# Kernel optimization log

Measured on AMD Instinct MI355X. Metric: run time of the kernel, lower is better.

The kernel has to match this reference:

```python
import jax, jax.numpy as jnp
import numpy as np

B, C, H, W = 1, 320, 64, 64
HEADS, DH = 8, 40            # inner_dim = 320
CTX_LEN, CTX_DIM = 77, 768
FF_MULT = 4
GN_GROUPS, GN_EPS = 32, 1e-6
LN_EPS = 1e-5
SCALE = DH ** -0.5
WSTD = 0.02


def setup_inputs() -> dict:
    key = jax.random.key(0)
    ks = iter(jax.random.split(key, 32))
    rn = lambda *s: jax.random.normal(next(ks), s, dtype=jnp.float32)
    D = HEADS * DH  # 320
    inp = {
        'hidden_states': rn(B, C, H, W),
        'encoder_hidden_states': rn(B, CTX_LEN, CTX_DIM),
        'gn_g': jnp.ones((C,), jnp.float32), 'gn_b': jnp.zeros((C,), jnp.float32),
        'pi_w': rn(C, D) * WSTD, 'pi_b': jnp.zeros((D,), jnp.float32),
        'n1_g': jnp.ones((D,), jnp.float32), 'n1_b': jnp.zeros((D,), jnp.float32),
        'a1_q': rn(D, D) * WSTD, 'a1_k': rn(D, D) * WSTD, 'a1_v': rn(D, D) * WSTD,
        'a1_o': rn(D, D) * WSTD, 'a1_ob': jnp.zeros((D,), jnp.float32),
        'n2_g': jnp.ones((D,), jnp.float32), 'n2_b': jnp.zeros((D,), jnp.float32),
        'a2_q': rn(D, D) * WSTD, 'a2_k': rn(CTX_DIM, D) * WSTD, 'a2_v': rn(CTX_DIM, D) * WSTD,
        'a2_o': rn(D, D) * WSTD, 'a2_ob': jnp.zeros((D,), jnp.float32),
        'n3_g': jnp.ones((D,), jnp.float32), 'n3_b': jnp.zeros((D,), jnp.float32),
        'ff_w1': rn(D, 2 * FF_MULT * D) * WSTD, 'ff_b1': jnp.zeros((2 * FF_MULT * D,), jnp.float32),
        'ff_w2': rn(FF_MULT * D, D) * WSTD, 'ff_b2': jnp.zeros((D,), jnp.float32),
        'po_w': rn(D, C) * WSTD, 'po_b': jnp.zeros((C,), jnp.float32),
    }
    return inp


def _group_norm(x, g, b):
    # x: [B,C,H,W]
    Bx, Cx, Hx, Wx = x.shape
    xr = x.reshape(Bx, GN_GROUPS, Cx // GN_GROUPS, Hx, Wx)
    mu = xr.mean(axis=(2, 3, 4), keepdims=True)
    var = xr.var(axis=(2, 3, 4), keepdims=True)
    xr = (xr - mu) * jax.lax.rsqrt(var + GN_EPS)
    x = xr.reshape(Bx, Cx, Hx, Wx)
    return x * g[None, :, None, None] + b[None, :, None, None]


def _layer_norm(x, g, b):
    mu = x.mean(-1, keepdims=True)
    var = x.var(-1, keepdims=True)
    return (x - mu) * jax.lax.rsqrt(var + LN_EPS) * g + b


def _attention(x, ctx, wq, wk, wv, wo, bo):
    # x: [B,S,D]; ctx: [B,T,Dc]. Same math as the torch sliced loop
    # (the 2-row slicing changes only execution order, not values).
    Bx, S, D = x.shape
    q = (x @ wq).reshape(Bx, S, HEADS, DH)
    k = (ctx @ wk).reshape(Bx, -1, HEADS, DH)
    v = (ctx @ wv).reshape(Bx, -1, HEADS, DH)
    s = jnp.einsum('bihd,bjhd->bhij', q, k) * SCALE
    p = jax.nn.softmax(s, axis=-1)
    o = jnp.einsum('bhij,bjhd->bihd', p, v).reshape(Bx, S, D)
    return o @ wo + bo


def reference(hidden_states, encoder_hidden_states, gn_g, gn_b, pi_w, pi_b,
              n1_g, n1_b, a1_q, a1_k, a1_v, a1_o, a1_ob,
              n2_g, n2_b, a2_q, a2_k, a2_v, a2_o, a2_ob,
              n3_g, n3_b, ff_w1, ff_b1, ff_w2, ff_b2, po_w, po_b):
    residual = hidden_states
    h = _group_norm(hidden_states, gn_g, gn_b)
    # proj_in: 1x1 conv == per-pixel linear; to [B, HW, D]
    h = jnp.einsum('bchw,cd->bhwd', h, pi_w) + pi_b
    Bx, Hx, Wx, D = h.shape
    h = h.reshape(Bx, Hx * Wx, D)

    # transformer block
    nh = _layer_norm(h, n1_g, n1_b)
    h = h + _attention(nh, nh, a1_q, a1_k, a1_v, a1_o, a1_ob)
    nh = _layer_norm(h, n2_g, n2_b)
    h = h + _attention(nh, encoder_hidden_states, a2_q, a2_k, a2_v, a2_o, a2_ob)
    nh = _layer_norm(h, n3_g, n3_b)
    hg = nh @ ff_w1 + ff_b1
    a, gate = jnp.split(hg, 2, axis=-1)  # GEGLU
    h = h + (a * jax.nn.gelu(gate, approximate=False)) @ ff_w2 + ff_b2

    # proj_out 1x1 conv then residual
    h = h.reshape(Bx, Hx, Wx, D)
    out = jnp.einsum('bhwd,dc->bchw', h, po_w) + po_b[None, :, None, None]
    return out + residual
```

## Files before the change

### kernel.cpp

```cpp
#include <hip/hip_runtime.h>

typedef __bf16 bf16x8 __attribute__((ext_vector_type(8)));
typedef __bf16 bf16x4 __attribute__((ext_vector_type(4)));
typedef __bf16 bf16x2 __attribute__((ext_vector_type(2)));
typedef float f32x4 __attribute__((ext_vector_type(4)));
typedef float f32x16 __attribute__((ext_vector_type(16)));

#define MFMA16(a, b, c) __builtin_amdgcn_mfma_f32_16x16x32_bf16(a, b, c, 0, 0, 0)
#define MFMA32(a, b, c) __builtin_amdgcn_mfma_f32_32x32x16_bf16(a, b, c, 0, 0, 0)

static constexpr float QSCALE = 0.15811388300841897f * 1.4426950408889634f;

__device__ __forceinline__ void gload16(const __bf16* g, __bf16* l) {
  __builtin_amdgcn_global_load_lds((const __attribute__((address_space(1))) void*)g,
                                   (__attribute__((address_space(3))) void*)l, 16, 0, 0);
}

__device__ __forceinline__ bf16x8 zero8() {
  bf16x8 z;
#pragma unroll
  for (int j = 0; j < 8; ++j) z[j] = (__bf16)0.0f;
  return z;
}

__device__ __forceinline__ float gelu_exact(float x) {
  return 0.5f * x * (1.0f + erff(x * 0.70710678118654752f));
}

__device__ __forceinline__ int vslot(int kk) {
  int G = kk >> 5, klo = kk & 31;
  int m = (klo >> 4) & 1, hik = (klo >> 2) & 1;
  int jj = (klo & 3) | (((klo >> 3) & 1) << 2);
  return (G << 5) | (m << 4) | (hik << 3) | jj;
}

struct WDesc { const float* src; __bf16* dst; int K; int N; int ldn; int noff; };
struct WTable { WDesc w[12]; };

__global__ __launch_bounds__(256) void wconv_kernel(WTable tab) {
  WDesc d = tab.w[blockIdx.y];
  int total = (d.K >> 3) * d.N;
  int idx = blockIdx.x * 256 + threadIdx.x;
  if (idx >= total) return;
  int kb = idx / d.N, n = idx - kb * d.N;
  bf16x8 o;
#pragma unroll
  for (int j = 0; j < 8; ++j) o[j] = (__bf16)d.src[(size_t)(kb * 8 + j) * d.N + n];
  *(bf16x8*)&d.dst[((size_t)kb * d.ldn + d.noff + n) * 8] = o;
}

__global__ __launch_bounds__(256) void gn_stats(const float* __restrict__ X,
                                                float* __restrict__ part) {
  int g = blockIdx.x >> 3, cid = blockIdx.x & 7;
  const float* base = X + (size_t)g * 40960 + (size_t)cid * 5120;
  int t = threadIdx.x;
  float s = 0.f, s2 = 0.f;
#pragma unroll
  for (int i = t; i < 1280; i += 256) {
    float4 v = ((const float4*)base)[i];
    s += v.x + v.y + v.z + v.w;
    s2 += v.x * v.x + v.y * v.y + v.z * v.z + v.w * v.w;
  }
#pragma unroll
  for (int off = 1; off < 64; off <<= 1) { s += __shfl_xor(s, off); s2 += __shfl_xor(s2, off); }
  __shared__ float rs[4], rs2[4];
  int wid = t >> 6, lane = t & 63;
  if (lane == 0) { rs[wid] = s; rs2[wid] = s2; }
  __syncthreads();
  if (t == 0) {
    part[blockIdx.x * 2] = rs[0] + rs[1] + rs[2] + rs[3];
    part[blockIdx.x * 2 + 1] = rs2[0] + rs2[1] + rs2[2] + rs2[3];
  }
}

__global__ __launch_bounds__(256) void gn_apply(const float* __restrict__ X,
                                                const float* __restrict__ part,
                                                const float* __restrict__ gg,
                                                const float* __restrict__ gb,
                                                __bf16* __restrict__ Y) {
  int i0 = (blockIdx.x * 256 + threadIdx.x) * 8;
  int c = i0 >> 12, px = i0 & 4095;
  int g = c / 10;
  float s = 0.f, s2 = 0.f;
#pragma unroll
  for (int j = 0; j < 8; ++j) { s += part[(g * 8 + j) * 2]; s2 += part[(g * 8 + j) * 2 + 1]; }
  float mu = s * (1.f / 40960.f);
  float rstd = rsqrtf(s2 * (1.f / 40960.f) - mu * mu + 1e-6f);
  float ga = gg[c] * rstd, bb = gb[c] - mu * ga;
  float4 a = *(const float4*)&X[i0];
  float4 b = *(const float4*)&X[i0 + 4];
  Y[(size_t)(px + 0) * 320 + c] = (__bf16)(a.x * ga + bb);
  Y[(size_t)(px + 1) * 320 + c] = (__bf16)(a.y * ga + bb);
  Y[(size_t)(px + 2) * 320 + c] = (__bf16)(a.z * ga + bb);
  Y[(size_t)(px + 3) * 320 + c] = (__bf16)(a.w * ga + bb);
  Y[(size_t)(px + 4) * 320 + c] = (__bf16)(b.x * ga + bb);
  Y[(size_t)(px + 5) * 320 + c] = (__bf16)(b.y * ga + bb);
  Y[(size_t)(px + 6) * 320 + c] = (__bf16)(b.z * ga + bb);
  Y[(size_t)(px + 7) * 320 + c] = (__bf16)(b.w * ga + bb);
}

__global__ __launch_bounds__(256) void ln_kernel(const float* __restrict__ X,
                                                 const float* __restrict__ g,
                                                 const float* __restrict__ b,
                                                 __bf16* __restrict__ Y) {
  int row = blockIdx.x * 4 + (threadIdx.x >> 6);
  int lane = threadIdx.x & 63;
  const float* x = X + (size_t)row * 320;
  float v[5];
  float s = 0.f;
#pragma unroll
  for (int i = 0; i < 5; ++i) { v[i] = x[lane + 64 * i]; s += v[i]; }
#pragma unroll
  for (int off = 1; off < 64; off <<= 1) s += __shfl_xor(s, off);
  float mu = s * (1.f / 320.f);
  float s2 = 0.f;
#pragma unroll
  for (int i = 0; i < 5; ++i) { float d = v[i] - mu; s2 += d * d; }
#pragma unroll
  for (int off = 1; off < 64; off <<= 1) s2 += __shfl_xor(s2, off);
  float rstd = rsqrtf(s2 * (1.f / 320.f) + 1e-5f);
#pragma unroll
  for (int i = 0; i < 5; ++i) {
    int c = lane + 64 * i;
    Y[(size_t)row * 320 + c] = (__bf16)((v[i] - mu) * rstd * g[c] + b[c]);
  }
}

template <int OM, bool HB, bool HR, bool QS, bool AH>
__global__ __launch_bounds__(256) void gemm64(const __bf16* __restrict__ A,
                                              const __bf16* __restrict__ Bt,
                                              const float* __restrict__ bias,
                                              const float* __restrict__ res,
                                              void* __restrict__ Cout,
                                              void* __restrict__ Cout2,
                                              int M, int N, int K) {
  __shared__ __align__(16) __bf16 sA[2][4096];
  __shared__ __align__(16) __bf16 sB[2][4096];
  int t = threadIdx.x, lane = t & 63, wid = t >> 6;
  int wr = wid >> 1, wc = wid & 1, kb4 = lane >> 4, l15 = lane & 15;
  int m0 = blockIdx.x * 64, n0 = blockIdx.y * 64;
  const size_t N8 = (size_t)N * 8;
  f32x4 acc[2][2] = {};
  int r0 = t >> 3, c0 = (t & 7) ^ (r0 & 7);

  auto stage = [&](int buf, int k0) {
    const __bf16 *ga0, *ga1;
    if (AH) {
      int kk = k0 + c0 * 8;
      int hh = kk / 40, dh = kk - hh * 40;
      ga0 = &A[((size_t)hh * 4096 + m0 + r0) * 40 + dh];
      ga1 = &A[((size_t)hh * 4096 + m0 + 32 + r0) * 40 + dh];
    } else {
      ga0 = &A[(size_t)(m0 + r0) * K + k0 + c0 * 8];
      ga1 = &A[(size_t)(m0 + 32 + r0) * K + k0 + c0 * 8];
    }
    gload16(ga0, &sA[buf][wid * 512]);
    gload16(ga1, &sA[buf][2048 + wid * 512]);
    gload16(&Bt[((size_t)(k0 >> 3) + wid) * N8 + (size_t)(n0 + lane) * 8], &sB[buf][wid * 512]);
    gload16(&Bt[((size_t)(k0 >> 3) + wid + 4) * N8 + (size_t)(n0 + lane) * 8], &sB[buf][2048 + wid * 512]);
  };
  stage(0, 0);
  __syncthreads();
  int cur = 0;
  for (int k0 = 0; k0 < K; k0 += 64) {
    if (k0 + 64 < K) stage(cur ^ 1, k0 + 64);
#pragma unroll
    for (int kk = 0; kk < 2; ++kk) {
      int c8 = kb4 + kk * 4;
      bf16x8 af[2], bfr[2];
#pragma unroll
      for (int fm = 0; fm < 2; ++fm) {
        int row = wr * 32 + fm * 16 + l15;
        af[fm] = *(const bf16x8*)&sA[cur][row * 64 + ((c8 * 8) ^ ((row & 7) << 3))];
      }
#pragma unroll
      for (int fn = 0; fn < 2; ++fn)
        bfr[fn] = *(const bf16x8*)&sB[cur][(c8 * 64 + wc * 32 + fn * 16 + l15) * 8];
#pragma unroll
      for (int fm = 0; fm < 2; ++fm)
#pragma unroll
        for (int fn = 0; fn < 2; ++fn) acc[fm][fn] = MFMA16(af[fm], bfr[fn], acc[fm][fn]);
    }
    __syncthreads();
    cur ^= 1;
  }
#pragma unroll
  for (int fm = 0; fm < 2; ++fm)
#pragma unroll
    for (int fn = 0; fn < 2; ++fn)
#pragma unroll
      for (int r = 0; r < 4; ++r) {
        int row = m0 + wr * 32 + fm * 16 + kb4 * 4 + r;
        int col = n0 + wc * 32 + fn * 16 + l15;
        float v = acc[fm][fn][r];
        if (HB) v += bias[col];
        if (OM == 3) {
          if (HR) v += res[(size_t)col * M + row];
          ((float*)Cout)[(size_t)col * M + row] = v;
        } else if (OM == 4) {
          int hh = col / 40, dh = col - hh * 40;
          __bf16* qp = (__bf16*)Cout + ((size_t)hh * 4096 + row) * 48 + dh;
          *qp = (__bf16)(QS ? v * QSCALE : v);
          if (dh >= 32) qp[8] = (__bf16)0.f;
        } else {
          if (HR) v += res[(size_t)row * N + col];
          if (OM == 0) {
            ((float*)Cout)[(size_t)row * N + col] = v;
          } else if (OM == 1) {
            ((__bf16*)Cout)[(size_t)row * N + col] = (__bf16)(QS ? v * QSCALE : v);
          } else {
            ((float*)Cout)[(size_t)row * N + col] = v;
            ((__bf16*)Cout2)[(size_t)row * N + col] = (__bf16)v;
          }
        }
      }
}

__global__ __launch_bounds__(256) void qkv_gemm(const __bf16* __restrict__ A,
                                                const __bf16* __restrict__ Bt,
                                                __bf16* __restrict__ Qh,
                                                __bf16* __restrict__ Khp,
                                                __bf16* __restrict__ Vtl) {
  __shared__ __align__(16) __bf16 sA[2][4096];
  __shared__ __align__(16) __bf16 sB[2][4096];
  int t = threadIdx.x, lane = t & 63, wid = t >> 6;
  int wr = wid >> 1, wc = wid & 1, kb4 = lane >> 4, l15 = lane & 15;
  int m0 = blockIdx.x * 64, n0 = blockIdx.y * 64;
  f32x4 acc[2][2] = {};
  int r0 = t >> 3, c0 = (t & 7) ^ (r0 & 7);

  auto stage = [&](int buf, int k0) {
    gload16(&A[(size_t)(m0 + r0) * 320 + k0 + c0 * 8], &sA[buf][wid * 512]);
    gload16(&A[(size_t)(m0 + 32 + r0) * 320 + k0 + c0 * 8], &sA[buf][2048 + wid * 512]);
    gload16(&Bt[((size_t)(k0 >> 3) + wid) * (960 * 8) + (size_t)(n0 + lane) * 8], &sB[buf][wid * 512]);
    gload16(&Bt[((size_t)(k0 >> 3) + wid + 4) * (960 * 8) + (size_t)(n0 + lane) * 8], &sB[buf][2048 + wid * 512]);
  };
  stage(0, 0);
  __syncthreads();
  int cur = 0;
  for (int k0 = 0; k0 < 320; k0 += 64) {
    if (k0 + 64 < 320) stage(cur ^ 1, k0 + 64);
#pragma unroll
    for (int kk = 0; kk < 2; ++kk) {
      int c8 = kb4 + kk * 4;
      bf16x8 af[2], bfr[2];
#pragma unroll
      for (int fm = 0; fm < 2; ++fm) {
        int row = wr * 32 + fm * 16 + l15;
        af[fm] = *(const bf16x8*)&sA[cur][row * 64 + ((c8 * 8) ^ ((row & 7) << 3))];
      }
#pragma unroll
      for (int fn = 0; fn < 2; ++fn)
        bfr[fn] = *(const bf16x8*)&sB[cur][(c8 * 64 + wc * 32 + fn * 16 + l15) * 8];
#pragma unroll
      for (int fm = 0; fm < 2; ++fm)
#pragma unroll
        for (int fn = 0; fn < 2; ++fn) acc[fm][fn] = MFMA16(af[fm], bfr[fn], acc[fm][fn]);
    }
    __syncthreads();
    cur ^= 1;
  }
#pragma unroll
  for (int fm = 0; fm < 2; ++fm)
#pragma unroll
    for (int fn = 0; fn < 2; ++fn)
#pragma unroll
      for (int r = 0; r < 4; ++r) {
        int row = m0 + wr * 32 + fm * 16 + kb4 * 4 + r;
        int col = n0 + wc * 32 + fn * 16 + l15;
        float v = acc[fm][fn][r];
        if (col < 320) {
          int hh = col / 40, dh = col - hh * 40;
          __bf16* qp = &Qh[((size_t)hh * 4096 + row) * 48 + dh];
          *qp = (__bf16)(v * QSCALE);
          if (dh >= 32) qp[8] = (__bf16)0.f;
        } else if (col < 640) {
          int d = col - 320;
          int hh = d / 40, dh = d - hh * 40;
          __bf16* kp = &Khp[((size_t)hh * 4096 + row) * 48 + dh];
          *kp = (__bf16)v;
          if (dh >= 32) kp[8] = (__bf16)0.f;
        } else {
          int d = col - 640;
          int hh = d / 40, dh = d - hh * 40;
          int kt = row >> 6;
          int slot = vslot(row & 63);
          int cidx = (slot & 7) | ((((slot >> 3) ^ dh) & 7) << 3);
          Vtl[(((size_t)hh * 64 + kt) * 40 + dh) * 64 + cidx] = (__bf16)v;
        }
      }
}

__global__ __launch_bounds__(256) void kv2_gemm(const float* __restrict__ Af,
                                                const __bf16* __restrict__ Bt,
                                                __bf16* __restrict__ Khp,
                                                __bf16* __restrict__ Vtl) {
  __shared__ __align__(16) __bf16 sA[2][4][64][8];
  __shared__ __align__(16) __bf16 sB[2][4][64][8];
  int t = threadIdx.x, lane = t & 63, wid = t >> 6;
  int wr = wid >> 1, wc = wid & 1, kb4 = lane >> 4, l15 = lane & 15;
  int m0 = blockIdx.x * 64, n0 = blockIdx.y * 64;
  int am = t & 63, ac8 = t >> 6;
  int bn = t & 63, bkb = t >> 6;
  f32x4 acc[2][2] = {};
  bf16x8 rA, rB;
  auto loadA = [&](int k0) -> bf16x8 {
    if (m0 + am < 77) {
      const float* src = &Af[(size_t)(m0 + am) * 768 + k0 + ac8 * 8];
      float4 x = *(const float4*)src;
      float4 y = *(const float4*)(src + 4);
      bf16x8 o;
      o[0] = (__bf16)x.x; o[1] = (__bf16)x.y; o[2] = (__bf16)x.z; o[3] = (__bf16)x.w;
      o[4] = (__bf16)y.x; o[5] = (__bf16)y.y; o[6] = (__bf16)y.z; o[7] = (__bf16)y.w;
      return o;
    }
    return zero8();
  };
  auto loadB = [&](int k0) {
    return *(const bf16x8*)&Bt[((size_t)(k0 >> 3) + bkb) * (640 * 8) + (size_t)(n0 + bn) * 8];
  };
  rA = loadA(0); rB = loadB(0);
  *(bf16x8*)&sA[0][ac8][am][0] = rA;
  *(bf16x8*)&sB[0][bkb][bn][0] = rB;
  __syncthreads();
  int cur = 0;
  for (int k0 = 0; k0 < 768; k0 += 32, cur ^= 1) {
    bool more = (k0 + 32) < 768;
    if (more) { rA = loadA(k0 + 32); rB = loadB(k0 + 32); }
    bf16x8 af[2], bfr[2];
#pragma unroll
    for (int fm = 0; fm < 2; ++fm) af[fm] = *(const bf16x8*)&sA[cur][kb4][wr * 32 + fm * 16 + l15][0];
#pragma unroll
    for (int fn = 0; fn < 2; ++fn) bfr[fn] = *(const bf16x8*)&sB[cur][kb4][wc * 32 + fn * 16 + l15][0];
#pragma unroll
    for (int fm = 0; fm < 2; ++fm)
#pragma unroll
      for (int fn = 0; fn < 2; ++fn) acc[fm][fn] = MFMA16(af[fm], bfr[fn], acc[fm][fn]);
    if (more) {
      *(bf16x8*)&sA[cur ^ 1][ac8][am][0] = rA;
      *(bf16x8*)&sB[cur ^ 1][bkb][bn][0] = rB;
    }
    __syncthreads();
  }
#pragma unroll
  for (int fm = 0; fm < 2; ++fm)
#pragma unroll
    for (int fn = 0; fn < 2; ++fn)
#pragma unroll
      for (int r = 0; r < 4; ++r) {
        int row = m0 + wr * 32 + fm * 16 + kb4 * 4 + r;
        int col = n0 + wc * 32 + fn * 16 + l15;
        float v = acc[fm][fn][r];
        if (col < 320) {
          int hh = col / 40, dh = col - hh * 40;
          __bf16* kp = &Khp[((size_t)hh * 128 + row) * 48 + dh];
          *kp = (__bf16)v;
          if (dh >= 32) kp[8] = (__bf16)0.f;
        } else {
          int d = col - 320;
          int hh = d / 40, dh = d - hh * 40;
          int kt = row >> 6;
          int slot = vslot(row & 63);
          int cidx = (slot & 7) | ((((slot >> 3) ^ dh) & 7) << 3);
          Vtl[(((size_t)hh * 2 + kt) * 40 + dh) * 64 + cidx] = (__bf16)v;
        }
      }
}

__global__ __launch_bounds__(256) void geglu64(const __bf16* __restrict__ A,
                                               const __bf16* __restrict__ Bt,
                                               const float* __restrict__ bias,
                                               __bf16* __restrict__ Out) {
  __shared__ __align__(16) __bf16 sA[2][4096];
  __shared__ __align__(16) __bf16 sB[2][4096];
  __shared__ __align__(16) __bf16 sBg[2][4096];
  int t = threadIdx.x, lane = t & 63, wid = t >> 6;
  int wr = wid >> 1, wc = wid & 1, kb4 = lane >> 4, l15 = lane & 15;
  int m0 = blockIdx.x * 64, n0 = blockIdx.y * 64;
  f32x4 acc_a[2][2] = {}, acc_g[2][2] = {};
  int r0 = t >> 3, c0 = (t & 7) ^ (r0 & 7);

  auto stage = [&](int buf, int k0) {
    gload16(&A[(size_t)(m0 + r0) * 320 + k0 + c0 * 8], &sA[buf][wid * 512]);
    gload16(&A[(size_t)(m0 + 32 + r0) * 320 + k0 + c0 * 8], &sA[buf][2048 + wid * 512]);
    gload16(&Bt[((size_t)(k0 >> 3) + wid) * (2560 * 8) + (size_t)(n0 + lane) * 8], &sB[buf][wid * 512]);
    gload16(&Bt[((size_t)(k0 >> 3) + wid + 4) * (2560 * 8) + (size_t)(n0 + lane) * 8], &sB[buf][2048 + wid * 512]);
    gload16(&Bt[((size_t)(k0 >> 3) + wid) * (2560 * 8) + (size_t)(1280 + n0 + lane) * 8], &sBg[buf][wid * 512]);
    gload16(&Bt[((size_t)(k0 >> 3) + wid + 4) * (2560 * 8) + (size_t)(1280 + n0 + lane) * 8], &sBg[buf][2048 + wid * 512]);
  };
  stage(0, 0);
  __syncthreads();
  int cur = 0;
  for (int k0 = 0; k0 < 320; k0 += 64) {
    if (k0 + 64 < 320) stage(cur ^ 1, k0 + 64);
#pragma unroll
    for (int kk = 0; kk < 2; ++kk) {
      int c8 = kb4 + kk * 4;
      bf16x8 af[2], bfa[2], bfg[2];
#pragma unroll
      for (int fm = 0; fm < 2; ++fm) {
        int row = wr * 32 + fm * 16 + l15;
        af[fm] = *(const bf16x8*)&sA[cur][row * 64 + ((c8 * 8) ^ ((row & 7) << 3))];
      }
#pragma unroll
      for (int fn = 0; fn < 2; ++fn) {
        bfa[fn] = *(const bf16x8*)&sB[cur][(c8 * 64 + wc * 32 + fn * 16 + l15) * 8];
        bfg[fn] = *(const bf16x8*)&sBg[cur][(c8 * 64 + wc * 32 + fn * 16 + l15) * 8];
      }
#pragma unroll
      for (int fm = 0; fm < 2; ++fm)
#pragma unroll
        for (int fn = 0; fn < 2; ++fn) {
          acc_a[fm][fn] = MFMA16(af[fm], bfa[fn], acc_a[fm][fn]);
          acc_g[fm][fn] = MFMA16(af[fm], bfg[fn], acc_g[fm][fn]);
        }
    }
    __syncthreads();
    cur ^= 1;
  }
#pragma unroll
  for (int fm = 0; fm < 2; ++fm)
#pragma unroll
    for (int fn = 0; fn < 2; ++fn)
#pragma unroll
      for (int r = 0; r < 4; ++r) {
        int row = m0 + wr * 32 + fm * 16 + kb4 * 4 + r;
        int col = n0 + wc * 32 + fn * 16 + l15;
        float a = acc_a[fm][fn][r] + bias[col];
        float g = acc_g[fm][fn][r] + bias[1280 + col];
        Out[(size_t)row * 1280 + col] = (__bf16)(a * gelu_exact(g));
      }
}

__global__ __launch_bounds__(512) void attn_kernel(const __bf16* __restrict__ Qh,
                                                   const __bf16* __restrict__ Khp,
                                                   const __bf16* __restrict__ Vtl,
                                                   __bf16* __restrict__ Oh,
                                                   int kv_len, int kvpad) {
  __shared__ __align__(16) char smem[48128];
  int t = threadIdx.x, lane = t & 63, wid = t >> 6;
  int zz = wid >> 2, kg = (wid >> 1) & 1, qg = wid & 1;
  int tl = t & 255, wv = wid & 3;
  int l31 = lane & 31, hi = lane >> 5;
  int h = blockIdx.y, q0 = blockIdx.x * 64;
  int q = q0 + qg * 32 + l31;
  int NT = kvpad >> 6;
  char* zbase = smem + zz * 22528;
  __bf16* sK  = (__bf16*)zbase;
  __bf16* sVs = (__bf16*)(zbase + 12288);
  __bf16* sVc = (__bf16*)(smem + 45056);
  for (int i = t; i < 1536; i += 512) sVc[i] = (i < 64) ? (__bf16)1.0f : (__bf16)0.0f;

  const __bf16* Kb = Khp + (size_t)h * kvpad * 48;
  const __bf16* Vb = Vtl + (size_t)h * NT * 2560;

  bf16x8 qf[3];
  {
    const __bf16* qrow = Qh + ((size_t)h * 4096 + q) * 48;
#pragma unroll
    for (int s = 0; s < 3; ++s) qf[s] = *(const bf16x8*)(qrow + s * 16 + hi * 8);
  }
  f32x16 o_lo = {}, o_hi = {};

  auto stage = [&](int buf, int k0) {
    const __bf16* kgp = Kb + (size_t)k0 * 48;
    __bf16* kd = sK + buf * 3072;
    gload16(kgp + tl * 8, kd + wv * 512);
    if (tl < 128) gload16(kgp + 2048 + tl * 8, kd + 2048 + wv * 512);
    const __bf16* vgp = Vb + (size_t)(k0 >> 6) * 2560;
    __bf16* vd = sVs + buf * 2560;
    gload16(vgp + tl * 8, vd + wv * 512);
    if (tl < 64) gload16(vgp + 2048 + tl * 8, vd + 2048);
  };

  int span = kvpad >> 1;
  int kstart = zz * span, ntl = span >> 6;
  stage(0, kstart);
  __syncthreads();
  int d7 = l31 & 7;
  for (int tile = 0; tile < ntl; ++tile) {
    int k0 = kstart + (tile << 6), cur = tile & 1;
    if (tile + 1 < ntl) stage(cur ^ 1, k0 + 64);
    const __bf16* K8 = sK + cur * 3072 + (kg * 32 + l31) * 48 + hi * 8;
    f32x16 s = {};
#pragma unroll
    for (int sl = 0; sl < 3; ++sl) {
      bf16x8 kf = *(const bf16x8*)(K8 + sl * 16);
      s = MFMA32(kf, qf[sl], s);
    }
    if (k0 + 64 > kv_len) {
#pragma unroll
      for (int r = 0; r < 16; ++r) {
        int klo = (r & 3) + 8 * (r >> 2) + 4 * hi;
        if (k0 + kg * 32 + klo >= kv_len) s[r] = -1e30f;
      }
    }
    bf16x8 p0, p1;
#pragma unroll
    for (int j = 0; j < 8; ++j) {
      p0[j] = (__bf16)exp2f(s[j]);
      p1[j] = (__bf16)exp2f(s[8 + j]);
    }
    const __bf16* Vlo = sVs + cur * 2560 + l31 * 64;
    const __bf16* Vhi = (l31 < 8) ? (sVs + cur * 2560 + (32 + l31) * 64)
                                  : (sVc + (l31 - 8) * 64);
#pragma unroll
    for (int m = 0; m < 2; ++m) {
      int blk = (4 * kg + 2 * m + hi) ^ d7;
      bf16x8 vlo = *(const bf16x8*)(Vlo + blk * 8);
      bf16x8 vhi = *(const bf16x8*)(Vhi + blk * 8);
      bf16x8 pm = (m == 0) ? p0 : p1;
      o_lo = MFMA32(vlo, pm, o_lo);
      o_hi = MFMA32(vhi, pm, o_hi);
    }
    __syncthreads();
  }
  float* sO = (float*)smem;
  int srcid = zz * 2 + kg;
  if (srcid != 0) {
    float* dst = sO + (((size_t)qg * 3 + (srcid - 1)) * 64 + lane) * 24;
#pragma unroll
    for (int r = 0; r < 16; ++r) dst[r] = o_lo[r];
#pragma unroll
    for (int r = 0; r < 4; ++r) dst[16 + r] = o_hi[r];
    dst[20] = o_hi[4];
  }
  __syncthreads();
  if (srcid == 0) {
#pragma unroll
    for (int src = 0; src < 3; ++src) {
      const float* sp = sO + (((size_t)qg * 3 + src) * 64 + lane) * 24;
#pragma unroll
      for (int r = 0; r < 16; ++r) o_lo[r] += sp[r];
#pragma unroll
      for (int r = 0; r < 4; ++r) o_hi[r] += sp[16 + r];
      o_hi[4] += sp[20];
    }
    float ls = __shfl(o_hi[4], l31);
    float inv = 1.0f / ls;
    __bf16* orow = Oh + ((size_t)h * 4096 + q) * 40;
#pragma unroll
    for (int r = 0; r < 16; r += 2) {
      int d = (r & 3) + 8 * (r >> 2) + 4 * hi;
      bf16x2 o2;
      o2[0] = (__bf16)(o_lo[r] * inv);
      o2[1] = (__bf16)(o_lo[r + 1] * inv);
      *(bf16x2*)(orow + d) = o2;
    }
#pragma unroll
    for (int r = 0; r < 4; r += 2) {
      int d = 32 + r + 4 * hi;
      bf16x2 o2;
      o2[0] = (__bf16)(o_hi[r] * inv);
      o2[1] = (__bf16)(o_hi[r + 1] * inv);
      *(bf16x2*)(orow + d) = o2;
    }
  }
}

extern "C" void kernel_launch(void* const* d_in, const int* in_sizes, int n_in,
                              void* d_out, int out_size, void* d_ws, size_t ws_size,
                              hipStream_t stream) {
  const float* hs    = (const float*)d_in[0];
  const float* ctx   = (const float*)d_in[1];
  const float* gn_g  = (const float*)d_in[2];
  const float* gn_b  = (const float*)d_in[3];
  const float* pi_w  = (const float*)d_in[4];
  const float* pi_b  = (const float*)d_in[5];
  const float* n1_g  = (const float*)d_in[6];
  const float* n1_b  = (const float*)d_in[7];
  const float* a1_q  = (const float*)d_in[8];
  const float* a1_k  = (const float*)d_in[9];
  const float* a1_v  = (const float*)d_in[10];
  const float* a1_o  = (const float*)d_in[11];
  const float* a1_ob = (const float*)d_in[12];
  const float* n2_g  = (const float*)d_in[13];
  const float* n2_b  = (const float*)d_in[14];
  const float* a2_q  = (const float*)d_in[15];
  const float* a2_k  = (const float*)d_in[16];
  const float* a2_v  = (const float*)d_in[17];
  const float* a2_o  = (const float*)d_in[18];
  const float* a2_ob = (const float*)d_in[19];
  const float* n3_g  = (const float*)d_in[20];
  const float* n3_b  = (const float*)d_in[21];
  const float* ff_w1 = (const float*)d_in[22];
  const float* ff_b1 = (const float*)d_in[23];
  const float* ff_w2 = (const float*)d_in[24];
  const float* ff_b2 = (const float*)d_in[25];
  const float* po_w  = (const float*)d_in[26];
  const float* po_b  = (const float*)d_in[27];

  char* p = (char*)d_ws;
  auto alloc = [&](size_t bytes) {
    char* r = p;
    p += (bytes + 255) & ~(size_t)255;
    return r;
  };
  __bf16* wPI  = (__bf16*)alloc((size_t)320 * 320 * 2);
  __bf16* wQKV = (__bf16*)alloc((size_t)320 * 960 * 2);
  __bf16* wO1  = (__bf16*)alloc((size_t)320 * 320 * 2);
  __bf16* wQ2  = (__bf16*)alloc((size_t)320 * 320 * 2);
  __bf16* wKV2 = (__bf16*)alloc((size_t)768 * 640 * 2);
  __bf16* wO2  = (__bf16*)alloc((size_t)320 * 320 * 2);
  __bf16* wFF1 = (__bf16*)alloc((size_t)320 * 2560 * 2);
  __bf16* wFF2 = (__bf16*)alloc((size_t)1280 * 320 * 2);
  __bf16* wPO  = (__bf16*)alloc((size_t)320 * 320 * 2);

  float*  gpart= (float*)alloc((size_t)256 * 2 * 4);
  __bf16* xg   = (__bf16*)alloc((size_t)4096 * 320 * 2);
  float*  h    = (float*)alloc((size_t)4096 * 320 * 4);
  __bf16* hb   = (__bf16*)alloc((size_t)4096 * 320 * 2);
  __bf16* nx   = (__bf16*)alloc((size_t)4096 * 320 * 2);
  __bf16* qh   = (__bf16*)alloc((size_t)8 * 4096 * 48 * 2);
  __bf16* khp  = (__bf16*)alloc((size_t)8 * 4096 * 48 * 2);
  __bf16* vtl  = (__bf16*)alloc((size_t)8 * 64 * 2560 * 2);
  __bf16* kh2  = (__bf16*)alloc((size_t)8 * 128 * 48 * 2);
  __bf16* vt2  = (__bf16*)alloc((size_t)8 * 2 * 2560 * 2);
  __bf16* oh   = (__bf16*)alloc((size_t)4096 * 320 * 2);
  __bf16* g    = (__bf16*)alloc((size_t)4096 * 1280 * 2);
  float*  outp = (float*)d_out;

  WTable tab;
  tab.w[0]  = WDesc{pi_w,  wPI,  320, 320, 320, 0};
  tab.w[1]  = WDesc{a1_q,  wQKV, 320, 320, 960, 0};
  tab.w[2]  = WDesc{a1_k,  wQKV, 320, 320, 960, 320};
  tab.w[3]  = WDesc{a1_v,  wQKV, 320, 320, 960, 640};
  tab.w[4]  = WDesc{a1_o,  wO1,  320, 320, 320, 0};
  tab.w[5]  = WDesc{a2_q,  wQ2,  320, 320, 320, 0};
  tab.w[6]  = WDesc{a2_k,  wKV2, 768, 320, 640, 0};
  tab.w[7]  = WDesc{a2_v,  wKV2, 768, 320, 640, 320};
  tab.w[8]  = WDesc{a2_o,  wO2,  320, 320, 320, 0};
  tab.w[9]  = WDesc{ff_w1, wFF1, 320, 2560, 2560, 0};
  tab.w[10] = WDesc{ff_w2, wFF2, 1280, 320, 320, 0};
  tab.w[11] = WDesc{po_w,  wPO,  320, 320, 320, 0};
  wconv_kernel<<<dim3(400, 12), 256, 0, stream>>>(tab);
  gn_stats<<<dim3(256), 256, 0, stream>>>(hs, gpart);
  gn_apply<<<dim3(640), 256, 0, stream>>>(hs, gpart, gn_g, gn_b, xg);
  gemm64<0, true, false, false, false><<<dim3(64, 5), 256, 0, stream>>>(xg, wPI, pi_b, nullptr, h, nullptr, 4096, 320, 320);
  ln_kernel<<<dim3(1024), 256, 0, stream>>>(h, n1_g, n1_b, nx);
  qkv_gemm<<<dim3(64, 15), 256, 0, stream>>>(nx, wQKV, qh, khp, vtl);
  attn_kernel<<<dim3(64, 8), 512, 0, stream>>>(qh, khp, vtl, oh, 4096, 4096);
  gemm64<0, true, true, false, true><<<dim3(64, 5), 256, 0, stream>>>(oh, wO1, a1_ob, h, h, nullptr, 4096, 320, 320);
  ln_kernel<<<dim3(1024), 256, 0, stream>>>(h, n2_g, n2_b, nx);
  gemm64<4, false, false, true, false><<<dim3(64, 5), 256, 0, stream>>>(nx, wQ2, nullptr, nullptr, qh, nullptr, 4096, 320, 320);
  kv2_gemm<<<dim3(2, 10), 256, 0, stream>>>(ctx, wKV2, kh2, vt2);
  attn_kernel<<<dim3(64, 8), 512, 0, stream>>>(qh, kh2, vt2, oh, 77, 128);
  gemm64<0, true, true, false, true><<<dim3(64, 5), 256, 0, stream>>>(oh, wO2, a2_ob, h, h, nullptr, 4096, 320, 320);
  ln_kernel<<<dim3(1024), 256, 0, stream>>>(h, n3_g, n3_b, nx);
  geglu64<<<dim3(64, 20), 256, 0, stream>>>(nx, wFF1, ff_b1, g);
  gemm64<2, true, true, false, false><<<dim3(64, 5), 256, 0, stream>>>(g, wFF2, ff_b2, h, h, hb, 4096, 320, 1280);
  gemm64<3, true, true, false, false><<<dim3(64, 5), 256, 0, stream>>>(hb, wPO, po_b, hs, outp, nullptr, 4096, 320, 320);
}
```

Before: 177.5 us.

## Halve attention block to 4 waves, each wave covering two query groups

The attention kernel drops from 512 to 256 threads per block. Each wave now processes both 32-query groups, so every K and V fragment read from LDS feeds twice as many MFMAs. K rows are padded from 48 to 56 elements, presumably to cut LDS bank conflicts on the K fragment reads; the producer GEMMs write the extra zero padding and the buffers grow to match. The cost is double the accumulator registers per wave and fewer waves per block to hide latency.

New measurement: 194.0 us. +9.3%, slower.

```diff
diff --git a/kernel.cpp b/kernel.cpp
--- a/kernel.cpp
+++ b/kernel.cpp
@@ -219,7 +219,7 @@
 __global__ __launch_bounds__(256) void qkv_gemm(const __bf16* __restrict__ A,
                                                 const __bf16* __restrict__ Bt,
                                                 __bf16* __restrict__ Qh,
-                                                __bf16* __restrict__ Khp,
+                                                __bf16* __restrict__ K56,
                                                 __bf16* __restrict__ Vtl) {
   __shared__ __align__(16) __bf16 sA[2][4096];
   __shared__ __align__(16) __bf16 sB[2][4096];
@@ -277,9 +277,9 @@
         } else if (col < 640) {
           int d = col - 320;
           int hh = d / 40, dh = d - hh * 40;
-          __bf16* kp = &Khp[((size_t)hh * 4096 + row) * 48 + dh];
+          __bf16* kp = &K56[((size_t)hh * 4096 + row) * 56 + dh];
           *kp = (__bf16)v;
-          if (dh >= 32) kp[8] = (__bf16)0.f;
+          if (dh >= 32) { kp[8] = (__bf16)0.f; kp[16] = (__bf16)0.f; }
         } else {
           int d = col - 640;
           int hh = d / 40, dh = d - hh * 40;
@@ -293,7 +293,7 @@
 
 __global__ __launch_bounds__(256) void kv2_gemm(const float* __restrict__ Af,
                                                 const __bf16* __restrict__ Bt,
-                                                __bf16* __restrict__ Khp,
+                                                __bf16* __restrict__ K56,
                                                 __bf16* __restrict__ Vtl) {
   __shared__ __align__(16) __bf16 sA[2][4][64][8];
   __shared__ __align__(16) __bf16 sB[2][4][64][8];
@@ -353,9 +353,9 @@
         float v = acc[fm][fn][r];
         if (col < 320) {
           int hh = col / 40, dh = col - hh * 40;
-          __bf16* kp = &Khp[((size_t)hh * 128 + row) * 48 + dh];
+          __bf16* kp = &K56[((size_t)hh * 128 + row) * 56 + dh];
           *kp = (__bf16)v;
-          if (dh >= 32) kp[8] = (__bf16)0.f;
+          if (dh >= 32) { kp[8] = (__bf16)0.f; kp[16] = (__bf16)0.f; }
         } else {
           int d = col - 320;
           int hh = d / 40, dh = d - hh * 40;
@@ -432,45 +432,47 @@
       }
 }
 
-__global__ __launch_bounds__(512) void attn_kernel(const __bf16* __restrict__ Qh,
-                                                   const __bf16* __restrict__ Khp,
+__global__ __launch_bounds__(256) void attn_kernel(const __bf16* __restrict__ Qh,
+                                                   const __bf16* __restrict__ K56,
                                                    const __bf16* __restrict__ Vtl,
                                                    __bf16* __restrict__ Oh,
                                                    int kv_len, int kvpad) {
-  __shared__ __align__(16) char smem[48128];
+  __shared__ __align__(16) char smem[52224];
   int t = threadIdx.x, lane = t & 63, wid = t >> 6;
-  int zz = wid >> 2, kg = (wid >> 1) & 1, qg = wid & 1;
-  int tl = t & 255, wv = wid & 3;
+  int zz = wid >> 1, kg = wid & 1;
   int l31 = lane & 31, hi = lane >> 5;
   int h = blockIdx.y, q0 = blockIdx.x * 64;
-  int q = q0 + qg * 32 + l31;
   int NT = kvpad >> 6;
-  char* zbase = smem + zz * 22528;
+  char* zbase = smem + zz * 24576;
   __bf16* sK  = (__bf16*)zbase;
-  __bf16* sVs = (__bf16*)(zbase + 12288);
-  __bf16* sVc = (__bf16*)(smem + 45056);
-  for (int i = t; i < 1536; i += 512) sVc[i] = (i < 64) ? (__bf16)1.0f : (__bf16)0.0f;
-
-  const __bf16* Kb = Khp + (size_t)h * kvpad * 48;
+  __bf16* sVs = (__bf16*)(zbase + 14336);
+  __bf16* sVc = (__bf16*)(smem + 49152);
+  for (int i = t; i < 1536; i += 256) sVc[i] = (i < 64) ? (__bf16)1.0f : (__bf16)0.0f;
+
+  const __bf16* Kb = K56 + (size_t)h * kvpad * 56;
   const __bf16* Vb = Vtl + (size_t)h * NT * 2560;
 
-  bf16x8 qf[3];
-  {
-    const __bf16* qrow = Qh + ((size_t)h * 4096 + q) * 48;
-#pragma unroll
-    for (int s = 0; s < 3; ++s) qf[s] = *(const bf16x8*)(qrow + s * 16 + hi * 8);
-  }
-  f32x16 o_lo = {}, o_hi = {};
+  bf16x8 qf[2][3];
+#pragma unroll
+  for (int g = 0; g < 2; ++g) {
+    const __bf16* qrow = Qh + ((size_t)h * 4096 + q0 + g * 32 + l31) * 48;
+#pragma unroll
+    for (int s = 0; s < 3; ++s) qf[g][s] = *(const bf16x8*)(qrow + s * 16 + hi * 8);
+  }
+  f32x16 oL0 = {}, oH0 = {}, oL1 = {}, oH1 = {};
 
   auto stage = [&](int buf, int k0) {
-    const __bf16* kgp = Kb + (size_t)k0 * 48;
-    __bf16* kd = sK + buf * 3072;
-    gload16(kgp + tl * 8, kd + wv * 512);
-    if (tl < 128) gload16(kgp + 2048 + tl * 8, kd + 2048 + wv * 512);
+    const __bf16* kgp = Kb + (size_t)k0 * 56;
+    __bf16* kd = sK + buf * 3584;
+    gload16(kgp + (kg * 64 + lane) * 8, kd + kg * 512);
+    gload16(kgp + (128 + kg * 64 + lane) * 8, kd + 1024 + kg * 512);
+    gload16(kgp + (256 + kg * 64 + lane) * 8, kd + 2048 + kg * 512);
+    if (kg == 0) gload16(kgp + (384 + lane) * 8, kd + 3072);
     const __bf16* vgp = Vb + (size_t)(k0 >> 6) * 2560;
     __bf16* vd = sVs + buf * 2560;
-    gload16(vgp + tl * 8, vd + wv * 512);
-    if (tl < 64) gload16(vgp + 2048 + tl * 8, vd + 2048);
+    gload16(vgp + (kg * 64 + lane) * 8, vd + kg * 512);
+    gload16(vgp + (128 + kg * 64 + lane) * 8, vd + 1024 + kg * 512);
+    if (kg == 1) gload16(vgp + (256 + lane) * 8, vd + 2048);
   };
 
   int span = kvpad >> 1;
@@ -481,25 +483,30 @@
   for (int tile = 0; tile < ntl; ++tile) {
     int k0 = kstart + (tile << 6), cur = tile & 1;
     if (tile + 1 < ntl) stage(cur ^ 1, k0 + 64);
-    const __bf16* K8 = sK + cur * 3072 + (kg * 32 + l31) * 48 + hi * 8;
-    f32x16 s = {};
-#pragma unroll
-    for (int sl = 0; sl < 3; ++sl) {
-      bf16x8 kf = *(const bf16x8*)(K8 + sl * 16);
-      s = MFMA32(kf, qf[sl], s);
-    }
-    if (k0 + 64 > kv_len) {
-#pragma unroll
-      for (int r = 0; r < 16; ++r) {
-        int klo = (r & 3) + 8 * (r >> 2) + 4 * hi;
-        if (k0 + kg * 32 + klo >= kv_len) s[r] = -1e30f;
-      }
-    }
-    bf16x8 p0, p1;
-#pragma unroll
-    for (int j = 0; j < 8; ++j) {
-      p0[j] = (__bf16)exp2f(s[j]);
-      p1[j] = (__bf16)exp2f(s[8 + j]);
+    const __bf16* K8 = sK + cur * 3584 + (kg * 32 + l31) * 56 + hi * 8;
+    bf16x8 kf0 = *(const bf16x8*)(K8);
+    bf16x8 kf1 = *(const bf16x8*)(K8 + 16);
+    bf16x8 kf2 = *(const bf16x8*)(K8 + 32);
+    bool msk = (k0 + 64) > kv_len;
+    bf16x8 p[2][2];
+#pragma unroll
+    for (int g = 0; g < 2; ++g) {
+      f32x16 s = {};
+      s = MFMA32(kf0, qf[g][0], s);
+      s = MFMA32(kf1, qf[g][1], s);
+      s = MFMA32(kf2, qf[g][2], s);
+      if (msk) {
+#pragma unroll
+        for (int r = 0; r < 16; ++r) {
+          int klo = (r & 3) + 8 * (r >> 2) + 4 * hi;
+          if (k0 + kg * 32 + klo >= kv_len) s[r] = -1e30f;
+        }
+      }
+#pragma unroll
+      for (int j = 0; j < 8; ++j) {
+        p[g][0][j] = (__bf16)exp2f(s[j]);
+        p[g][1][j] = (__bf16)exp2f(s[8 + j]);
+      }
     }
     const __bf16* Vlo = sVs + cur * 2560 + l31 * 64;
     const __bf16* Vhi = (l31 < 8) ? (sVs + cur * 2560 + (32 + l31) * 64)
@@ -509,51 +516,62 @@
       int blk = (4 * kg + 2 * m + hi) ^ d7;
       bf16x8 vlo = *(const bf16x8*)(Vlo + blk * 8);
       bf16x8 vhi = *(const bf16x8*)(Vhi + blk * 8);
-      bf16x8 pm = (m == 0) ? p0 : p1;
-      o_lo = MFMA32(vlo, pm, o_lo);
-      o_hi = MFMA32(vhi, pm, o_hi);
+      oL0 = MFMA32(vlo, p[0][m], oL0);
+      oH0 = MFMA32(vhi, p[0][m], oH0);
+      oL1 = MFMA32(vlo, p[1][m], oL1);
+      oH1 = MFMA32(vhi, p[1][m], oH1);
     }
     __syncthreads();
   }
   float* sO = (float*)smem;
   int srcid = zz * 2 + kg;
   if (srcid != 0) {
-    float* dst = sO + (((size_t)qg * 3 + (srcid - 1)) * 64 + lane) * 24;
-#pragma unroll
-    for (int r = 0; r < 16; ++r) dst[r] = o_lo[r];
-#pragma unroll
-    for (int r = 0; r < 4; ++r) dst[16 + r] = o_hi[r];
-    dst[20] = o_hi[4];
+#pragma unroll
+    for (int g = 0; g < 2; ++g) {
+      float* dst = sO + (((size_t)g * 3 + (srcid - 1)) * 64 + lane) * 22;
+      const f32x16& ol = g ? oL1 : oL0;
+      const f32x16& oh = g ? oH1 : oH0;
+#pragma unroll
+      for (int r = 0; r < 16; ++r) dst[r] = ol[r];
+#pragma unroll
+      for (int r = 0; r < 4; ++r) dst[16 + r] = oh[r];
+      dst[20] = oh[4];
+    }
   }
   __syncthreads();
   if (srcid == 0) {
 #pragma unroll
-    for (int src = 0; src < 3; ++src) {
-      const float* sp = sO + (((size_t)qg * 3 + src) * 64 + lane) * 24;
-#pragma unroll
-      for (int r = 0; r < 16; ++r) o_lo[r] += sp[r];
-#pragma unroll
-      for (int r = 0; r < 4; ++r) o_hi[r] += sp[16 + r];
-      o_hi[4] += sp[20];
-    }
-    float ls = __shfl(o_hi[4], l31);
-    float inv = 1.0f / ls;
-    __bf16* orow = Oh + ((size_t)h * 4096 + q) * 40;
-#pragma unroll
-    for (int r = 0; r < 16; r += 2) {
-      int d = (r & 3) + 8 * (r >> 2) + 4 * hi;
-      bf16x2 o2;
-      o2[0] = (__bf16)(o_lo[r] * inv);
-      o2[1] = (__bf16)(o_lo[r + 1] * inv);
-      *(bf16x2*)(orow + d) = o2;
-    }
-#pragma unroll
-    for (int r = 0; r < 4; r += 2) {
-      int d = 32 + r + 4 * hi;
-      bf16x2 o2;
-      o2[0] = (__bf16)(o_hi[r] * inv);
-      o2[1] = (__bf16)(o_hi[r + 1] * inv);
-      *(bf16x2*)(orow + d) = o2;
+    for (int g = 0; g < 2; ++g) {
+      f32x16 ol = g ? oL1 : oL0;
+      f32x16 oh = g ? oH1 : oH0;
+#pragma unroll
+      for (int src = 0; src < 3; ++src) {
+        const float* sp = sO + (((size_t)g * 3 + src) * 64 + lane) * 22;
+#pragma unroll
+        for (int r = 0; r < 16; ++r) ol[r] += sp[r];
+#pragma unroll
+        for (int r = 0; r < 4; ++r) oh[r] += sp[16 + r];
+        oh[4] += sp[20];
+      }
+      float ls = __shfl(oh[4], l31);
+      float inv = 1.0f / ls;
+      __bf16* orow = Oh + ((size_t)h * 4096 + q0 + g * 32 + l31) * 40;
+#pragma unroll
+      for (int r = 0; r < 16; r += 2) {
+        int d = (r & 3) + 8 * (r >> 2) + 4 * hi;
+        bf16x2 o2;
+        o2[0] = (__bf16)(ol[r] * inv);
+        o2[1] = (__bf16)(ol[r + 1] * inv);
+        *(bf16x2*)(orow + d) = o2;
+      }
+#pragma unroll
+      for (int r = 0; r < 4; r += 2) {
+        int d = 32 + r + 4 * hi;
+        bf16x2 o2;
+        o2[0] = (__bf16)(oh[r] * inv);
+        o2[1] = (__bf16)(oh[r + 1] * inv);
+        *(bf16x2*)(orow + d) = o2;
+      }
     }
   }
 }
@@ -612,9 +630,9 @@
   __bf16* hb   = (__bf16*)alloc((size_t)4096 * 320 * 2);
   __bf16* nx   = (__bf16*)alloc((size_t)4096 * 320 * 2);
   __bf16* qh   = (__bf16*)alloc((size_t)8 * 4096 * 48 * 2);
-  __bf16* khp  = (__bf16*)alloc((size_t)8 * 4096 * 48 * 2);
+  __bf16* k56  = (__bf16*)alloc((size_t)8 * 4096 * 56 * 2);
   __bf16* vtl  = (__bf16*)alloc((size_t)8 * 64 * 2560 * 2);
-  __bf16* kh2  = (__bf16*)alloc((size_t)8 * 128 * 48 * 2);
+  __bf16* k562 = (__bf16*)alloc((size_t)8 * 128 * 56 * 2);
   __bf16* vt2  = (__bf16*)alloc((size_t)8 * 2 * 2560 * 2);
   __bf16* oh   = (__bf16*)alloc((size_t)4096 * 320 * 2);
   __bf16* g    = (__bf16*)alloc((size_t)4096 * 1280 * 2);
@@ -638,13 +656,13 @@
   gn_apply<<<dim3(640), 256, 0, stream>>>(hs, gpart, gn_g, gn_b, xg);
   gemm64<0, true, false, false, false><<<dim3(64, 5), 256, 0, stream>>>(xg, wPI, pi_b, nullptr, h, nullptr, 4096, 320, 320);
   ln_kernel<<<dim3(1024), 256, 0, stream>>>(h, n1_g, n1_b, nx);
-  qkv_gemm<<<dim3(64, 15), 256, 0, stream>>>(nx, wQKV, qh, khp, vtl);
-  attn_kernel<<<dim3(64, 8), 512, 0, stream>>>(qh, khp, vtl, oh, 4096, 4096);
+  qkv_gemm<<<dim3(64, 15), 256, 0, stream>>>(nx, wQKV, qh, k56, vtl);
+  attn_kernel<<<dim3(64, 8), 256, 0, stream>>>(qh, k56, vtl, oh, 4096, 4096);
   gemm64<0, true, true, false, true><<<dim3(64, 5), 256, 0, stream>>>(oh, wO1, a1_ob, h, h, nullptr, 4096, 320, 320);
   ln_kernel<<<dim3(1024), 256, 0, stream>>>(h, n2_g, n2_b, nx);
   gemm64<4, false, false, true, false><<<dim3(64, 5), 256, 0, stream>>>(nx, wQ2, nullptr, nullptr, qh, nullptr, 4096, 320, 320);
-  kv2_gemm<<<dim3(2, 10), 256, 0, stream>>>(ctx, wKV2, kh2, vt2);
-  attn_kernel<<<dim3(64, 8), 512, 0, stream>>>(qh, kh2, vt2, oh, 77, 128);
+  kv2_gemm<<<dim3(2, 10), 256, 0, stream>>>(ctx, wKV2, k562, vt2);
+  attn_kernel<<<dim3(64, 8), 256, 0, stream>>>(qh, k562, vt2, oh, 77, 128);
   gemm64<0, true, true, false, true><<<dim3(64, 5), 256, 0, stream>>>(oh, wO2, a2_ob, h, h, nullptr, 4096, 320, 320);
   ln_kernel<<<dim3(1024), 256, 0, stream>>>(h, n3_g, n3_b, nx);
   geglu64<<<dim3(64, 20), 256, 0, stream>>>(nx, wFF1, ff_b1, g);
```

## Use 32-row GEMM tiles for N=320 projections and pad K rows to 56

Applied to the files above, without the earlier changes.

Adds a gemm32 kernel with 32x64 tiles and switches all the N=320 projection GEMMs to it. The grid doubles from 320 to 640 blocks, which fills the CUs better at the cost of less A/B reuse per block. Separately, the attention K buffer row stride goes from 48 to 56 elements, and the LDS layout and staging are adjusted to match. The padding is meant to reduce LDS bank conflicts on K fragment reads, in exchange for more K bytes loaded and more shared memory per block.

New measurement: 175.5 us. Within noise of the previous version (-1.1%).

```diff
diff --git a/kernel.cpp b/kernel.cpp
--- a/kernel.cpp
+++ b/kernel.cpp
@@ -216,10 +216,90 @@
       }
 }
 
+template <int OM, bool HB, bool HR, bool QS, bool AH>
+__global__ __launch_bounds__(256) void gemm32(const __bf16* __restrict__ A,
+                                              const __bf16* __restrict__ Bt,
+                                              const float* __restrict__ bias,
+                                              const float* __restrict__ res,
+                                              void* __restrict__ Cout,
+                                              void* __restrict__ Cout2,
+                                              int M, int N, int K) {
+  __shared__ __align__(16) __bf16 sA[2][2048];
+  __shared__ __align__(16) __bf16 sB[2][4096];
+  int t = threadIdx.x, lane = t & 63, wid = t >> 6;
+  int wr = wid >> 1, wc = wid & 1, kb4 = lane >> 4, l15 = lane & 15;
+  int m0 = blockIdx.x * 32, n0 = blockIdx.y * 64;
+  const size_t N8 = (size_t)N * 8;
+  f32x4 acc[2] = {};
+  int r0 = t >> 3, c0 = (t & 7) ^ (r0 & 7);
+
+  auto stage = [&](int buf, int k0) {
+    const __bf16* ga0;
+    if (AH) {
+      int kk = k0 + c0 * 8;
+      int hh = kk / 40, dh = kk - hh * 40;
+      ga0 = &A[((size_t)hh * 4096 + m0 + r0) * 40 + dh];
+    } else {
+      ga0 = &A[(size_t)(m0 + r0) * K + k0 + c0 * 8];
+    }
+    gload16(ga0, &sA[buf][wid * 512]);
+    gload16(&Bt[((size_t)(k0 >> 3) + wid) * N8 + (size_t)(n0 + lane) * 8], &sB[buf][wid * 512]);
+    gload16(&Bt[((size_t)(k0 >> 3) + wid + 4) * N8 + (size_t)(n0 + lane) * 8], &sB[buf][2048 + wid * 512]);
+  };
+  stage(0, 0);
+  __syncthreads();
+  int cur = 0;
+  for (int k0 = 0; k0 < K; k0 += 64) {
+    if (k0 + 64 < K) stage(cur ^ 1, k0 + 64);
+#pragma unroll
+    for (int kk = 0; kk < 2; ++kk) {
+      int c8 = kb4 + kk * 4;
+      int row = wr * 16 + l15;
+      bf16x8 af = *(const bf16x8*)&sA[cur][row * 64 + ((c8 * 8) ^ ((row & 7) << 3))];
+      bf16x8 bfr[2];
+#pragma unroll
+      for (int fn = 0; fn < 2; ++fn)
+        bfr[fn] = *(const bf16x8*)&sB[cur][(c8 * 64 + wc * 32 + fn * 16 + l15) * 8];
+#pragma unroll
+      for (int fn = 0; fn < 2; ++fn) acc[fn] = MFMA16(af, bfr[fn], acc[fn]);
+    }
+    __syncthreads();
+    cur ^= 1;
+  }
+#pragma unroll
+  for (int fn = 0; fn < 2; ++fn)
+#pragma unroll
+    for (int r = 0; r < 4; ++r) {
+      int row = m0 + wr * 16 + kb4 * 4 + r;
+      int col = n0 + wc * 32 + fn * 16 + l15;
+      float v = acc[fn][r];
+      if (HB) v += bias[col];
+      if (OM == 3) {
+        if (HR) v += res[(size_t)col * M + row];
+        ((float*)Cout)[(size_t)col * M + row] = v;
+      } else if (OM == 4) {
+        int hh = col / 40, dh = col - hh * 40;
+        __bf16* qp = (__bf16*)Cout + ((size_t)hh * 4096 + row) * 48 + dh;
+        *qp = (__bf16)(QS ? v * QSCALE : v);
+        if (dh >= 32) qp[8] = (__bf16)0.f;
+      } else {
+        if (HR) v += res[(size_t)row * N + col];
+        if (OM == 0) {
+          ((float*)Cout)[(size_t)row * N + col] = v;
+        } else if (OM == 1) {
+          ((__bf16*)Cout)[(size_t)row * N + col] = (__bf16)(QS ? v * QSCALE : v);
+        } else {
+          ((float*)Cout)[(size_t)row * N + col] = v;
+          ((__bf16*)Cout2)[(size_t)row * N + col] = (__bf16)v;
+        }
+      }
+    }
+}
+
 __global__ __launch_bounds__(256) void qkv_gemm(const __bf16* __restrict__ A,
                                                 const __bf16* __restrict__ Bt,
                                                 __bf16* __restrict__ Qh,
-                                                __bf16* __restrict__ Khp,
+                                                __bf16* __restrict__ K56,
                                                 __bf16* __restrict__ Vtl) {
   __shared__ __align__(16) __bf16 sA[2][4096];
   __shared__ __align__(16) __bf16 sB[2][4096];
@@ -277,9 +357,9 @@
         } else if (col < 640) {
           int d = col - 320;
           int hh = d / 40, dh = d - hh * 40;
-          __bf16* kp = &Khp[((size_t)hh * 4096 + row) * 48 + dh];
+          __bf16* kp = &K56[((size_t)hh * 4096 + row) * 56 + dh];
           *kp = (__bf16)v;
-          if (dh >= 32) kp[8] = (__bf16)0.f;
+          if (dh >= 32) { kp[8] = (__bf16)0.f; kp[16] = (__bf16)0.f; }
         } else {
           int d = col - 640;
           int hh = d / 40, dh = d - hh * 40;
@@ -293,7 +373,7 @@
 
 __global__ __launch_bounds__(256) void kv2_gemm(const float* __restrict__ Af,
                                                 const __bf16* __restrict__ Bt,
-                                                __bf16* __restrict__ Khp,
+                                                __bf16* __restrict__ K56,
                                                 __bf16* __restrict__ Vtl) {
   __shared__ __align__(16) __bf16 sA[2][4][64][8];
   __shared__ __align__(16) __bf16 sB[2][4][64][8];
@@ -353,9 +433,9 @@
         float v = acc[fm][fn][r];
         if (col < 320) {
           int hh = col / 40, dh = col - hh * 40;
-          __bf16* kp = &Khp[((size_t)hh * 128 + row) * 48 + dh];
+          __bf16* kp = &K56[((size_t)hh * 128 + row) * 56 + dh];
           *kp = (__bf16)v;
-          if (dh >= 32) kp[8] = (__bf16)0.f;
+          if (dh >= 32) { kp[8] = (__bf16)0.f; kp[16] = (__bf16)0.f; }
         } else {
           int d = col - 320;
           int hh = d / 40, dh = d - hh * 40;
@@ -433,11 +513,11 @@
 }
 
 __global__ __launch_bounds__(512) void attn_kernel(const __bf16* __restrict__ Qh,
-                                                   const __bf16* __restrict__ Khp,
+                                                   const __bf16* __restrict__ K56,
                                                    const __bf16* __restrict__ Vtl,
                                                    __bf16* __restrict__ Oh,
                                                    int kv_len, int kvpad) {
-  __shared__ __align__(16) char smem[48128];
+  __shared__ __align__(16) char smem[52224];
   int t = threadIdx.x, lane = t & 63, wid = t >> 6;
   int zz = wid >> 2, kg = (wid >> 1) & 1, qg = wid & 1;
   int tl = t & 255, wv = wid & 3;
@@ -445,13 +525,13 @@
   int h = blockIdx.y, q0 = blockIdx.x * 64;
   int q = q0 + qg * 32 + l31;
   int NT = kvpad >> 6;
-  char* zbase = smem + zz * 22528;
+  char* zbase = smem + zz * 24576;
   __bf16* sK  = (__bf16*)zbase;
-  __bf16* sVs = (__bf16*)(zbase + 12288);
-  __bf16* sVc = (__bf16*)(smem + 45056);
+  __bf16* sVs = (__bf16*)(zbase + 14336);
+  __bf16* sVc = (__bf16*)(smem + 49152);
   for (int i = t; i < 1536; i += 512) sVc[i] = (i < 64) ? (__bf16)1.0f : (__bf16)0.0f;
 
-  const __bf16* Kb = Khp + (size_t)h * kvpad * 48;
+  const __bf16* Kb = K56 + (size_t)h * kvpad * 56;
   const __bf16* Vb = Vtl + (size_t)h * NT * 2560;
 
   bf16x8 qf[3];
@@ -463,14 +543,14 @@
   f32x16 o_lo = {}, o_hi = {};
 
   auto stage = [&](int buf, int k0) {
-    const __bf16* kgp = Kb + (size_t)k0 * 48;
-    __bf16* kd = sK + buf * 3072;
+    const __bf16* kgp = Kb + (size_t)k0 * 56;
+    __bf16* kd = sK + buf * 3584;
     gload16(kgp + tl * 8, kd + wv * 512);
-    if (tl < 128) gload16(kgp + 2048 + tl * 8, kd + 2048 + wv * 512);
+    if (wv < 3) gload16(kgp + 2048 + wv * 512 + lane * 8, kd + 2048 + wv * 512);
     const __bf16* vgp = Vb + (size_t)(k0 >> 6) * 2560;
     __bf16* vd = sVs + buf * 2560;
     gload16(vgp + tl * 8, vd + wv * 512);
-    if (tl < 64) gload16(vgp + 2048 + tl * 8, vd + 2048);
+    if (wv == 3) gload16(vgp + 2048 + lane * 8, vd + 2048);
   };
 
   int span = kvpad >> 1;
@@ -481,13 +561,11 @@
   for (int tile = 0; tile < ntl; ++tile) {
     int k0 = kstart + (tile << 6), cur = tile & 1;
     if (tile + 1 < ntl) stage(cur ^ 1, k0 + 64);
-    const __bf16* K8 = sK + cur * 3072 + (kg * 32 + l31) * 48 + hi * 8;
+    const __bf16* K8 = sK + cur * 3584 + (kg * 32 + l31) * 56 + hi * 8;
     f32x16 s = {};
-#pragma unroll
-    for (int sl = 0; sl < 3; ++sl) {
-      bf16x8 kf = *(const bf16x8*)(K8 + sl * 16);
-      s = MFMA32(kf, qf[sl], s);
-    }
+    s = MFMA32(*(const bf16x8*)(K8), qf[0], s);
+    s = MFMA32(*(const bf16x8*)(K8 + 16), qf[1], s);
+    s = MFMA32(*(const bf16x8*)(K8 + 32), qf[2], s);
     if (k0 + 64 > kv_len) {
 #pragma unroll
       for (int r = 0; r < 16; ++r) {
@@ -612,9 +690,9 @@
   __bf16* hb   = (__bf16*)alloc((size_t)4096 * 320 * 2);
   __bf16* nx   = (__bf16*)alloc((size_t)4096 * 320 * 2);
   __bf16* qh   = (__bf16*)alloc((size_t)8 * 4096 * 48 * 2);
-  __bf16* khp  = (__bf16*)alloc((size_t)8 * 4096 * 48 * 2);
+  __bf16* k56  = (__bf16*)alloc((size_t)8 * 4096 * 56 * 2);
   __bf16* vtl  = (__bf16*)alloc((size_t)8 * 64 * 2560 * 2);
-  __bf16* kh2  = (__bf16*)alloc((size_t)8 * 128 * 48 * 2);
+  __bf16* k562 = (__bf16*)alloc((size_t)8 * 128 * 56 * 2);
   __bf16* vt2  = (__bf16*)alloc((size_t)8 * 2 * 2560 * 2);
   __bf16* oh   = (__bf16*)alloc((size_t)4096 * 320 * 2);
   __bf16* g    = (__bf16*)alloc((size_t)4096 * 1280 * 2);
@@ -636,18 +714,18 @@
   wconv_kernel<<<dim3(400, 12), 256, 0, stream>>>(tab);
   gn_stats<<<dim3(256), 256, 0, stream>>>(hs, gpart);
   gn_apply<<<dim3(640), 256, 0, stream>>>(hs, gpart, gn_g, gn_b, xg);
-  gemm64<0, true, false, false, false><<<dim3(64, 5), 256, 0, stream>>>(xg, wPI, pi_b, nullptr, h, nullptr, 4096, 320, 320);
+  gemm32<0, true, false, false, false><<<dim3(128, 5), 256, 0, stream>>>(xg, wPI, pi_b, nullptr, h, nullptr, 4096, 320, 320);
   ln_kernel<<<dim3(1024), 256, 0, stream>>>(h, n1_g, n1_b, nx);
-  qkv_gemm<<<dim3(64, 15), 256, 0, stream>>>(nx, wQKV, qh, khp, vtl);
-  attn_kernel<<<dim3(64, 8), 512, 0, stream>>>(qh, khp, vtl, oh, 4096, 4096);
-  gemm64<0, true, true, false, true><<<dim3(64, 5), 256, 0, stream>>>(oh, wO1, a1_ob, h, h, nullptr, 4096, 320, 320);
+  qkv_gemm<<<dim3(64, 15), 256, 0, stream>>>(nx, wQKV, qh, k56, vtl);
+  attn_kernel<<<dim3(64, 8), 512, 0, stream>>>(qh, k56, vtl, oh, 4096, 4096);
+  gemm32<0, true, true, false, true><<<dim3(128, 5), 256, 0, stream>>>(oh, wO1, a1_ob, h, h, nullptr, 4096, 320, 320);
   ln_kernel<<<dim3(1024), 256, 0, stream>>>(h, n2_g, n2_b, nx);
-  gemm64<4, false, false, true, false><<<dim3(64, 5), 256, 0, stream>>>(nx, wQ2, nullptr, nullptr, qh, nullptr, 4096, 320, 320);
-  kv2_gemm<<<dim3(2, 10), 256, 0, stream>>>(ctx, wKV2, kh2, vt2);
-  attn_kernel<<<dim3(64, 8), 512, 0, stream>>>(qh, kh2, vt2, oh, 77, 128);
-  gemm64<0, true, true, false, true><<<dim3(64, 5), 256, 0, stream>>>(oh, wO2, a2_ob, h, h, nullptr, 4096, 320, 320);
+  gemm32<4, false, false, true, false><<<dim3(128, 5), 256, 0, stream>>>(nx, wQ2, nullptr, nullptr, qh, nullptr, 4096, 320, 320);
+  kv2_gemm<<<dim3(2, 10), 256, 0, stream>>>(ctx, wKV2, k562, vt2);
+  attn_kernel<<<dim3(64, 8), 512, 0, stream>>>(qh, k562, vt2, oh, 77, 128);
+  gemm32<0, true, true, false, true><<<dim3(128, 5), 256, 0, stream>>>(oh, wO2, a2_ob, h, h, nullptr, 4096, 320, 320);
   ln_kernel<<<dim3(1024), 256, 0, stream>>>(h, n3_g, n3_b, nx);
   geglu64<<<dim3(64, 20), 256, 0, stream>>>(nx, wFF1, ff_b1, g);
-  gemm64<2, true, true, false, false><<<dim3(64, 5), 256, 0, stream>>>(g, wFF2, ff_b2, h, h, hb, 4096, 320, 1280);
-  gemm64<3, true, true, false, false><<<dim3(64, 5), 256, 0, stream>>>(hb, wPO, po_b, hs, outp, nullptr, 4096, 320, 320);
-}
+  gemm32<2, true, true, false, false><<<dim3(128, 5), 256, 0, stream>>>(g, wFF2, ff_b2, h, h, hb, 4096, 320, 1280);
+  gemm32<3, true, true, false, false><<<dim3(128, 5), 256, 0, stream>>>(hb, wPO, po_b, hs, outp, nullptr, 4096, 320, 320);
+}
```
